# Kernel optimization log

Hardware: AMD Instinct MI355X
Metric: run time of the kernel (lower is better)

The kernel has to match this reference:

```python
import jax, jax.numpy as jnp
import numpy as np

D_MODEL = 1024
HEADS = 16
D_FF = 2048
EPS = 1e-6


def _ln(z, alpha, beta):
    # Faithful to the repo's (buggy-looking) LayerNorm:
    # mu = z - mean; sigma = std + eps; out = (z - mu/sigma)*alpha + beta
    mean = jnp.mean(z, axis=-1, keepdims=True)
    std = jnp.std(z, axis=-1, keepdims=True, ddof=1)  # torch.std is unbiased
    return (z - (z - mean) / (std + EPS)) * alpha + beta


def setup_inputs() -> dict:
    key = jax.random.key(0)
    ks = jax.random.split(key, 16)
    B, S, D = 8, 1024, D_MODEL
    s = 0.02
    inp = {
        "x": jax.random.normal(ks[0], (B, S, D), dtype=jnp.float32),
        "mask": jax.random.randint(ks[1], (B, S), 0, 2, dtype=jnp.int32),
        "Wq": jax.random.normal(ks[2], (D, D), dtype=jnp.float32) * s,
        "bq": jnp.zeros((D,), dtype=jnp.float32),
        "Wk": jax.random.normal(ks[3], (D, D), dtype=jnp.float32) * s,
        "bk": jnp.zeros((D,), dtype=jnp.float32),
        "Wv": jax.random.normal(ks[4], (D, D), dtype=jnp.float32) * s,
        "bv": jnp.zeros((D,), dtype=jnp.float32),
        "Wo": jax.random.normal(ks[5], (D, D), dtype=jnp.float32) * s,
        "bo": jnp.zeros((D,), dtype=jnp.float32),
        "W1": jax.random.normal(ks[6], (D_FF, D), dtype=jnp.float32) * s,
        "b1": jnp.zeros((D_FF,), dtype=jnp.float32),
        "W2": jax.random.normal(ks[7], (D, D_FF), dtype=jnp.float32) * s,
        "b2": jnp.zeros((D,), dtype=jnp.float32),
        "alpha1": jnp.ones((D,), dtype=jnp.float32),
        "beta1": jnp.zeros((D,), dtype=jnp.float32),
        "alpha2": jnp.ones((D,), dtype=jnp.float32),
        "beta2": jnp.zeros((D,), dtype=jnp.float32),
    }
    return inp


def reference(x, mask, Wq, bq, Wk, bk, Wv, bv, Wo, bo, W1, b1, W2, b2,
              alpha1, beta1, alpha2, beta2):
    B, S, D = x.shape
    H, dk = HEADS, D // HEADS
    # QKV projections (torch Linear: y = x @ W.T + b), split heads -> [B,H,S,dk]
    Q = (x @ Wq.T + bq).reshape(B, S, H, dk).transpose(0, 2, 1, 3)
    K = (x @ Wk.T + bk).reshape(B, S, H, dk).transpose(0, 2, 1, 3)
    V = (x @ Wv.T + bv).reshape(B, S, H, dk).transpose(0, 2, 1, 3)
    scores = jnp.einsum('bhqd,bhkd->bhqk', Q, K) / jnp.sqrt(jnp.float32(dk))
    # faithful mask broadcast: [B,1,S,1] over query rows
    m = mask[:, None, :, None]
    scores = jnp.where(m == 0, jnp.float32(-1e9), scores)
    A = jax.nn.softmax(scores, axis=-1)
    O = jnp.einsum('bhqk,bhkd->bhqd', A, V).transpose(0, 2, 1, 3).reshape(B, S, D)
    attn_out = O @ Wo.T + bo
    x1 = _ln(x + attn_out, alpha1, beta1)
    h = jax.nn.relu(x1 @ W1.T + b1)
    ff = h @ W2.T + b2
    return _ln(x1 + ff, alpha2, beta2)
```

## Files before the change

### kernel.cpp

```cpp
#include <hip/hip_runtime.h>
#include <cstdint>
#include <cstddef>

#define D_MODEL 1024
#define HEADS   16
#define DKH     64
#define D_FF    2048
#define SEQ     1024
#define BATCH   8
#define MROWS   (BATCH*SEQ)
#define LN_EPS  1e-6f

typedef __bf16 bh8 __attribute__((ext_vector_type(8)));
typedef float  f32x4 __attribute__((ext_vector_type(4)));
typedef unsigned short us8 __attribute__((ext_vector_type(8)));

__device__ __forceinline__ unsigned short f2bf(float f) {
  union { float f; unsigned int u; } c; c.f = f;
  unsigned int u = c.u;
  u = u + 0x7fffu + ((u >> 16) & 1u);
  return (unsigned short)(u >> 16);
}
__device__ __forceinline__ float bf2f(unsigned short h) {
  union { unsigned int u; float f; } c; c.u = ((unsigned int)h) << 16;
  return c.f;
}

__device__ __forceinline__ bh8 as_bh8(us8 v) { return __builtin_bit_cast(bh8, v); }

__device__ __forceinline__ void gl16(const unsigned short* g, unsigned short* l) {
  __builtin_amdgcn_global_load_lds(
      (const __attribute__((address_space(1))) unsigned int*)g,
      (__attribute__((address_space(3))) unsigned int*)l, 16, 0, 0);
}

__global__ void cast_bf16_k(const float* __restrict__ in, unsigned short* __restrict__ out, int n4) {
  int i = blockIdx.x * blockDim.x + threadIdx.x;
  if (i < n4) {
    float4 v = ((const float4*)in)[i];
    ushort4 o;
    o.x = f2bf(v.x); o.y = f2bf(v.y); o.z = f2bf(v.z); o.w = f2bf(v.w);
    ((ushort4*)out)[i] = o;
  }
}

__global__ void castw_k(const float* __restrict__ wq, const float* __restrict__ wk,
                        const float* __restrict__ wv, const float* __restrict__ wo,
                        const float* __restrict__ w1, const float* __restrict__ w2,
                        unsigned short* __restrict__ oqkv, unsigned short* __restrict__ oo,
                        unsigned short* __restrict__ o1, unsigned short* __restrict__ o2) {
  int i = blockIdx.x * blockDim.x + threadIdx.x;
  const int seg = i >> 18;
  const int loc = i & 262143;
  const float* src; unsigned short* dst; int il, ol;
  if (seg < 3)      { src = (seg == 0) ? wq : (seg == 1) ? wk : wv; dst = oqkv; il = loc; ol = seg * 262144 + loc; }
  else if (seg == 3){ src = wo; dst = oo; il = loc; ol = loc; }
  else if (seg < 6) { src = w1; dst = o1; il = (seg - 4) * 262144 + loc; ol = il; }
  else              { src = w2; dst = o2; il = (seg - 6) * 262144 + loc; ol = il; }
  float4 v = ((const float4*)src)[il];
  ushort4 o;
  o.x = f2bf(v.x); o.y = f2bf(v.y); o.z = f2bf(v.z); o.w = f2bf(v.w);
  ((ushort4*)dst)[ol] = o;
}

#define BM 128
#define BN 128
#define BK 64

template<int EPI>
__global__ __launch_bounds__(256)
void gemm_bt(const unsigned short* __restrict__ A, const unsigned short* __restrict__ Bw,
             const float* __restrict__ b0, const float* __restrict__ b1f,
             const float* __restrict__ b2f, const float* __restrict__ resid,
             void* __restrict__ out0, void* __restrict__ out1, void* __restrict__ out2,
             int M, int N, int K)
{
  __shared__ __align__(16) unsigned short As[2][BM * BK];
  __shared__ __align__(16) unsigned short Bs[2][BM * BK];

  const int tid  = threadIdx.x;
  const int lane = tid & 63;
  const int w    = tid >> 6;
  const int wr   = w >> 1;
  const int wc   = w & 1;
  const int l15  = lane & 15;
  const int l4   = lane >> 4;

  const int gx  = gridDim.x;
  const int nwg = gx * gridDim.y;
  int lin = blockIdx.y * gx + blockIdx.x;
  lin = (lin & 7) * (nwg >> 3) + (lin >> 3);
  const int brow = (lin / gx) * BM;
  const int bcol = (lin % gx) * BN;

  int rowj[4], offj[4];
  #pragma unroll
  for (int j = 0; j < 4; ++j) {
    const int c = tid + j * 256;
    rowj[j] = c >> 3;
    offj[j] = ((c & 7) ^ ((c >> 3) & 7)) * 8;
  }

  const unsigned short* Ag = A  + (size_t)brow * K;
  const unsigned short* Bg = Bw + (size_t)bcol * K;

  auto stage = [&](int bsel, int k0) {
    #pragma unroll
    for (int j = 0; j < 4; ++j)
      gl16(Ag + (size_t)rowj[j] * K + k0 + offj[j], &As[bsel][(tid + j * 256) * 8]);
    #pragma unroll
    for (int j = 0; j < 4; ++j)
      gl16(Bg + (size_t)rowj[j] * K + k0 + offj[j], &Bs[bsel][(tid + j * 256) * 8]);
  };

  const int NT = K / BK;
  stage(0, 0);
  stage(1, BK);

  f32x4 acc[4][4] = {};
  const int sw7 = l15 & 7;

  for (int t = 0; t < NT; ++t) {
    const int cur = t & 1;
    if (t + 1 < NT) { asm volatile("s_waitcnt vmcnt(8)" ::: "memory"); }
    else            { asm volatile("s_waitcnt vmcnt(0)" ::: "memory"); }
    __builtin_amdgcn_s_barrier();

    us8 aF[2][4], bF[2][4];
    #pragma unroll
    for (int h = 0; h < 2; ++h) {
      const int slot = ((h * 4 + l4) ^ sw7) * 8;
      #pragma unroll
      for (int mi = 0; mi < 4; ++mi)
        aF[h][mi] = *(const us8*)(&As[cur][(wr * 64 + mi * 16 + l15) * BK + slot]);
      #pragma unroll
      for (int ni = 0; ni < 4; ++ni)
        bF[h][ni] = *(const us8*)(&Bs[cur][(wc * 64 + ni * 16 + l15) * BK + slot]);
    }
    asm volatile("s_waitcnt lgkmcnt(0)" ::: "memory");
    __builtin_amdgcn_s_barrier();

    if (t + 2 < NT) stage(cur, (t + 2) * BK);

    #pragma unroll
    for (int h = 0; h < 2; ++h)
      #pragma unroll
      for (int mi = 0; mi < 4; ++mi)
        #pragma unroll
        for (int ni = 0; ni < 4; ++ni)
          acc[mi][ni] = __builtin_amdgcn_mfma_f32_16x16x32_bf16(
              as_bh8(aF[h][mi]), as_bh8(bF[h][ni]), acc[mi][ni], 0, 0, 0);
  }

  const int tt = bcol >> 10;
  #pragma unroll
  for (int mi = 0; mi < 4; ++mi) {
    #pragma unroll
    for (int ni = 0; ni < 4; ++ni) {
      const int gcol = bcol + wc * 64 + ni * 16 + l15;
      if (EPI == 4) {
        const int ccol = gcol & 1023;
        const float bv = ((tt == 0) ? b0 : (tt == 1) ? b1f : b2f)[ccol];
        const int grow0 = brow + wr * 64 + mi * 16 + l4 * 4;
        if (tt == 2) {
          const int bb = grow0 >> 10;
          const int s0 = grow0 & 1023;
          ushort4 pk;
          pk.x = f2bf(acc[mi][ni][0] + bv);
          pk.y = f2bf(acc[mi][ni][1] + bv);
          pk.z = f2bf(acc[mi][ni][2] + bv);
          pk.w = f2bf(acc[mi][ni][3] + bv);
          *(ushort4*)((unsigned short*)out2 + ((size_t)bb * D_MODEL + ccol) * SEQ + s0) = pk;
        } else {
          unsigned short* ob = (unsigned short*)(tt == 0 ? out0 : out1);
          #pragma unroll
          for (int v = 0; v < 4; ++v)
            ob[(size_t)(grow0 + v) * D_MODEL + ccol] = f2bf(acc[mi][ni][v] + bv);
        }
      } else {
        const float bv = b0[gcol];
        #pragma unroll
        for (int v = 0; v < 4; ++v) {
          const int grow = brow + wr * 64 + mi * 16 + l4 * 4 + v;
          float val = acc[mi][ni][v] + bv;
          if (EPI == 3) val = fmaxf(val, 0.0f);
          if (EPI == 2) {
            val += resid[(size_t)grow * N + gcol];
            ((float*)out0)[(size_t)grow * N + gcol] = val;
          } else {
            ((unsigned short*)out0)[(size_t)grow * N + gcol] = f2bf(val);
          }
        }
      }
    }
  }
}

__global__ __launch_bounds__(256)
void attn_k(const unsigned short* __restrict__ Q, const unsigned short* __restrict__ Kb,
            const unsigned short* __restrict__ Vt, const int* __restrict__ mask,
            unsigned short* __restrict__ O)
{
  __shared__ __align__(16) unsigned short Ks[2][64][64];
  __shared__ __align__(16) unsigned short Vs[2][64][64];
  __shared__ __align__(16) unsigned short Pl[4][16][88];

  const int bid = (blockIdx.x & 7) * 256 + (blockIdx.x >> 3);
  const int qc = bid & 15;
  const int h  = (bid >> 4) & 15;
  const int b  = bid >> 8;
  const int q0 = qc * 64;

  const int tid  = threadIdx.x;
  const int lane = tid & 63;
  const int w    = tid >> 6;
  const int l15  = lane & 15;
  const int l4   = lane >> 4;

  const int c0 = tid, c1 = tid + 256;
  const int kr0 = c0 >> 3, ke0 = ((c0 & 7) ^ (kr0 & 7)) * 8;
  const int kr1 = c1 >> 3, ke1 = ((c1 & 7) ^ (kr1 & 7)) * 8;

  const unsigned short* Kbase = Kb + ((size_t)b * SEQ) * D_MODEL + h * DKH;
  const unsigned short* Vbase = Vt + ((size_t)b * D_MODEL + h * DKH) * SEQ;

  const unsigned short* qp = Q + ((size_t)(b * SEQ + q0 + w * 16 + l15)) * D_MODEL + h * DKH + l4 * 8;
  const float qs = mask[b * SEQ + q0 + w * 16 + l15] ? 0.18033688011112042f : 0.0f;
  us8 q0r = *(const us8*)qp;
  us8 q1r = *(const us8*)(qp + 32);
  us8 q0s, q1s;
  #pragma unroll
  for (int j = 0; j < 8; ++j) {
    q0s[j] = f2bf(bf2f(q0r[j]) * qs);
    q1s[j] = f2bf(bf2f(q1r[j]) * qs);
  }
  const bh8 aQ0 = as_bh8(q0s);
  const bh8 aQ1 = as_bh8(q1s);

  float l[4] = {0.f, 0.f, 0.f, 0.f};
  f32x4 oacc[4] = {};

  gl16(Kbase + (size_t)kr0 * D_MODEL + ke0, &Ks[0][0][0] + c0 * 8);
  gl16(Kbase + (size_t)kr1 * D_MODEL + ke1, &Ks[0][0][0] + c1 * 8);
  gl16(Vbase + (size_t)kr0 * SEQ + ke0,     &Vs[0][0][0] + c0 * 8);
  gl16(Vbase + (size_t)kr1 * SEQ + ke1,     &Vs[0][0][0] + c1 * 8);
  __syncthreads();

  for (int t = 0; t < 16; ++t) {
    const int cur = t & 1;
    if (t < 15) {
      const int kv = (t + 1) * 64;
      gl16(Kbase + (size_t)(kv + kr0) * D_MODEL + ke0, &Ks[cur ^ 1][0][0] + c0 * 8);
      gl16(Kbase + (size_t)(kv + kr1) * D_MODEL + ke1, &Ks[cur ^ 1][0][0] + c1 * 8);
      gl16(Vbase + (size_t)kr0 * SEQ + kv + ke0,       &Vs[cur ^ 1][0][0] + c0 * 8);
      gl16(Vbase + (size_t)kr1 * SEQ + kv + ke1,       &Vs[cur ^ 1][0][0] + c1 * 8);
    }

    f32x4 s[4];
    #pragma unroll
    for (int kt = 0; kt < 4; ++kt) {
      const int row = kt * 16 + l15;
      const int swz = l15 & 7;
      bh8 bK0 = as_bh8(*(const us8*)(&Ks[cur][row][(l4 ^ swz) * 8]));
      bh8 bK1 = as_bh8(*(const us8*)(&Ks[cur][row][((4 + l4) ^ swz) * 8]));
      f32x4 t0 = {0.f, 0.f, 0.f, 0.f};
      t0 = __builtin_amdgcn_mfma_f32_16x16x32_bf16(aQ0, bK0, t0, 0, 0, 0);
      t0 = __builtin_amdgcn_mfma_f32_16x16x32_bf16(aQ1, bK1, t0, 0, 0, 0);
      s[kt] = t0;
    }

    #pragma unroll
    for (int v = 0; v < 4; ++v) {
      float ls = 0.f;
      #pragma unroll
      for (int kt = 0; kt < 4; ++kt) {
        float e = __builtin_amdgcn_exp2f(s[kt][v]);
        s[kt][v] = e;
        ls += e;
      }
      l[v] += ls;
    }

    #pragma unroll
    for (int kt = 0; kt < 4; ++kt)
      #pragma unroll
      for (int v = 0; v < 4; ++v)
        Pl[w][l4 * 4 + v][kt * 16 + l15] = f2bf(s[kt][v]);

    #pragma unroll
    for (int ks = 0; ks < 2; ++ks) {
      bh8 aP = as_bh8(*(const us8*)(&Pl[w][l15][ks * 32 + l4 * 8]));
      #pragma unroll
      for (int ds = 0; ds < 4; ++ds) {
        const int row = ds * 16 + l15;
        bh8 bV = as_bh8(*(const us8*)(&Vs[cur][row][((ks * 4 + l4) ^ (l15 & 7)) * 8]));
        oacc[ds] = __builtin_amdgcn_mfma_f32_16x16x32_bf16(aP, bV, oacc[ds], 0, 0, 0);
      }
    }
    __syncthreads();
  }

  #pragma unroll
  for (int v = 0; v < 4; ++v) {
    float lv = l[v];
    #pragma unroll
    for (int d = 1; d < 16; d <<= 1) lv += __shfl_xor(lv, d, 64);
    const float inv = 1.0f / lv;
    const int q = q0 + w * 16 + l4 * 4 + v;
    #pragma unroll
    for (int ds = 0; ds < 4; ++ds)
      O[((size_t)(b * SEQ + q)) * D_MODEL + h * DKH + ds * 16 + l15] =
          f2bf(oacc[ds][v] * inv);
  }
}

template<bool WBF>
__global__ __launch_bounds__(256)
void ln_k(const float* __restrict__ z, const float* __restrict__ alpha,
          const float* __restrict__ beta, float* __restrict__ yf,
          unsigned short* __restrict__ yb)
{
  const int row = blockIdx.x;
  const int tid = threadIdx.x;
  const float4 v = ((const float4*)(z + (size_t)row * D_MODEL))[tid];
  float s  = v.x + v.y + v.z + v.w;
  float ss = v.x * v.x + v.y * v.y + v.z * v.z + v.w * v.w;
  #pragma unroll
  for (int d = 1; d < 64; d <<= 1) {
    s  += __shfl_xor(s, d, 64);
    ss += __shfl_xor(ss, d, 64);
  }
  __shared__ float red[8];
  const int w = tid >> 6;
  if ((tid & 63) == 0) { red[w * 2] = s; red[w * 2 + 1] = ss; }
  __syncthreads();
  const float S  = red[0] + red[2] + red[4] + red[6];
  const float SS = red[1] + red[3] + red[5] + red[7];
  const float mean = S * (1.0f / 1024.0f);
  float var = (SS - 1024.0f * mean * mean) * (1.0f / 1023.0f);
  var = fmaxf(var, 0.0f);
  const float invd = 1.0f / (sqrtf(var) + LN_EPS);

  const float4 a  = ((const float4*)alpha)[tid];
  const float4 be = ((const float4*)beta)[tid];
  float4 y;
  y.x = (v.x - (v.x - mean) * invd) * a.x + be.x;
  y.y = (v.y - (v.y - mean) * invd) * a.y + be.y;
  y.z = (v.z - (v.z - mean) * invd) * a.z + be.z;
  y.w = (v.w - (v.w - mean) * invd) * a.w + be.w;
  ((float4*)(yf + (size_t)row * D_MODEL))[tid] = y;
  if (WBF) {
    ushort4 pk;
    pk.x = f2bf(y.x); pk.y = f2bf(y.y); pk.z = f2bf(y.z); pk.w = f2bf(y.w);
    ((ushort4*)(yb + (size_t)row * D_MODEL))[tid] = pk;
  }
}

extern "C" void kernel_launch(void* const* d_in, const int* in_sizes, int n_in,
                              void* d_out, int out_size, void* d_ws, size_t ws_size,
                              hipStream_t stream) {
  const float* x    = (const float*)d_in[0];
  const int*   mask = (const int*)d_in[1];
  const float* Wq = (const float*)d_in[2];  const float* bq = (const float*)d_in[3];
  const float* Wk = (const float*)d_in[4];  const float* bk = (const float*)d_in[5];
  const float* Wv = (const float*)d_in[6];  const float* bv = (const float*)d_in[7];
  const float* Wo = (const float*)d_in[8];  const float* bo = (const float*)d_in[9];
  const float* W1 = (const float*)d_in[10]; const float* b1 = (const float*)d_in[11];
  const float* W2 = (const float*)d_in[12]; const float* b2 = (const float*)d_in[13];
  const float* alpha1 = (const float*)d_in[14]; const float* beta1 = (const float*)d_in[15];
  const float* alpha2 = (const float*)d_in[16]; const float* beta2 = (const float*)d_in[17];
  (void)in_sizes; (void)n_in; (void)out_size; (void)ws_size;

  char* ws = (char*)d_ws;
  const size_t MB = (size_t)1 << 20;
  unsigned short* xb    = (unsigned short*)(ws + 0 * MB);
  unsigned short* Wqkvb = (unsigned short*)(ws + 16 * MB);
  unsigned short* Wob   = (unsigned short*)(ws + 22 * MB);
  unsigned short* W1b   = (unsigned short*)(ws + 24 * MB);
  unsigned short* W2b   = (unsigned short*)(ws + 28 * MB);
  unsigned short* Qb    = (unsigned short*)(ws + 32 * MB);
  unsigned short* Kb2   = (unsigned short*)(ws + 48 * MB);
  unsigned short* Vt    = (unsigned short*)(ws + 64 * MB);
  unsigned short* Ob    = (unsigned short*)(ws + 80 * MB);
  float*          zf    = (float*)(ws + 96 * MB);
  float*          x1f   = (float*)(ws + 128 * MB);
  unsigned short* x1b   = (unsigned short*)(ws + 160 * MB);
  unsigned short* hb    = Qb;

  cast_bf16_k<<<8192, 256, 0, stream>>>(x, xb, MROWS * D_MODEL / 4);
  castw_k<<<8192, 256, 0, stream>>>(Wq, Wk, Wv, Wo, W1, W2, Wqkvb, Wob, W1b, W2b);

  gemm_bt<4><<<dim3(24, 64), 256, 0, stream>>>(xb, Wqkvb, bq, bk, bv, nullptr,
                                               Qb, Kb2, Vt, MROWS, 3072, D_MODEL);

  attn_k<<<BATCH * HEADS * (SEQ / 64), 256, 0, stream>>>(Qb, Kb2, Vt, mask, Ob);

  gemm_bt<2><<<dim3(8, 64), 256, 0, stream>>>(Ob, Wob, bo, nullptr, nullptr, x,
                                              zf, nullptr, nullptr, MROWS, D_MODEL, D_MODEL);
  ln_k<true><<<MROWS, 256, 0, stream>>>(zf, alpha1, beta1, x1f, x1b);

  gemm_bt<3><<<dim3(16, 64), 256, 0, stream>>>(x1b, W1b, b1, nullptr, nullptr, nullptr,
                                               hb, nullptr, nullptr, MROWS, D_FF, D_MODEL);
  gemm_bt<2><<<dim3(8, 64), 256, 0, stream>>>(hb, W2b, b2, nullptr, nullptr, x1f,
                                              zf, nullptr, nullptr, MROWS, D_MODEL, D_FF);

  ln_k<false><<<MROWS, 256, 0, stream>>>(zf, alpha2, beta2, (float*)d_out, nullptr);
}
```

Baseline: 296.7 us.

## Prefetch KV two tiles ahead and load LDS fragments into registers early

The attention kernel now stages the first two K/V tiles up front and, inside the loop, waits with a partial vmcnt so that one tile's global loads stay in flight. Each iteration first copies all K and V fragments for the current tile from LDS into registers, then hits a barrier and reuses that buffer for the tile two steps ahead. This gives global loads more time to land, and the MFMA work runs from registers. In exchange each iteration has two barriers and uses more registers for the fragments, and the vmcnt count relies on gl16 being exactly four outstanding loads per stage.

```diff
diff --git a/kernel.cpp b/kernel.cpp
--- a/kernel.cpp
+++ b/kernel.cpp
@@ -240,32 +240,49 @@
   float l[4] = {0.f, 0.f, 0.f, 0.f};
   f32x4 oacc[4] = {};
 
-  gl16(Kbase + (size_t)kr0 * D_MODEL + ke0, &Ks[0][0][0] + c0 * 8);
-  gl16(Kbase + (size_t)kr1 * D_MODEL + ke1, &Ks[0][0][0] + c1 * 8);
-  gl16(Vbase + (size_t)kr0 * SEQ + ke0,     &Vs[0][0][0] + c0 * 8);
-  gl16(Vbase + (size_t)kr1 * SEQ + ke1,     &Vs[0][0][0] + c1 * 8);
-  __syncthreads();
+  auto stageKV = [&](int bsel, int kv) {
+    gl16(Kbase + (size_t)(kv + kr0) * D_MODEL + ke0, &Ks[bsel][0][0] + c0 * 8);
+    gl16(Kbase + (size_t)(kv + kr1) * D_MODEL + ke1, &Ks[bsel][0][0] + c1 * 8);
+    gl16(Vbase + (size_t)kr0 * SEQ + kv + ke0,       &Vs[bsel][0][0] + c0 * 8);
+    gl16(Vbase + (size_t)kr1 * SEQ + kv + ke1,       &Vs[bsel][0][0] + c1 * 8);
+  };
+
+  stageKV(0, 0);
+  stageKV(1, 64);
+
+  const int swz = l15 & 7;
 
   for (int t = 0; t < 16; ++t) {
     const int cur = t & 1;
-    if (t < 15) {
-      const int kv = (t + 1) * 64;
-      gl16(Kbase + (size_t)(kv + kr0) * D_MODEL + ke0, &Ks[cur ^ 1][0][0] + c0 * 8);
-      gl16(Kbase + (size_t)(kv + kr1) * D_MODEL + ke1, &Ks[cur ^ 1][0][0] + c1 * 8);
-      gl16(Vbase + (size_t)kr0 * SEQ + kv + ke0,       &Vs[cur ^ 1][0][0] + c0 * 8);
-      gl16(Vbase + (size_t)kr1 * SEQ + kv + ke1,       &Vs[cur ^ 1][0][0] + c1 * 8);
-    }
-
-    f32x4 s[4];
+    if (t + 1 < 16) { asm volatile("s_waitcnt vmcnt(4)" ::: "memory"); }
+    else            { asm volatile("s_waitcnt vmcnt(0)" ::: "memory"); }
+    __builtin_amdgcn_s_barrier();
+
+    us8 kF[4][2], vF[2][4];
     #pragma unroll
     for (int kt = 0; kt < 4; ++kt) {
       const int row = kt * 16 + l15;
-      const int swz = l15 & 7;
-      bh8 bK0 = as_bh8(*(const us8*)(&Ks[cur][row][(l4 ^ swz) * 8]));
-      bh8 bK1 = as_bh8(*(const us8*)(&Ks[cur][row][((4 + l4) ^ swz) * 8]));
+      kF[kt][0] = *(const us8*)(&Ks[cur][row][(l4 ^ swz) * 8]);
+      kF[kt][1] = *(const us8*)(&Ks[cur][row][((4 + l4) ^ swz) * 8]);
+    }
+    #pragma unroll
+    for (int ks = 0; ks < 2; ++ks)
+      #pragma unroll
+      for (int ds = 0; ds < 4; ++ds) {
+        const int row = ds * 16 + l15;
+        vF[ks][ds] = *(const us8*)(&Vs[cur][row][((ks * 4 + l4) ^ swz) * 8]);
+      }
+    asm volatile("s_waitcnt lgkmcnt(0)" ::: "memory");
+    __builtin_amdgcn_s_barrier();
+
+    if (t + 2 < 16) stageKV(cur, (t + 2) * 64);
+
+    f32x4 s[4];
+    #pragma unroll
+    for (int kt = 0; kt < 4; ++kt) {
       f32x4 t0 = {0.f, 0.f, 0.f, 0.f};
-      t0 = __builtin_amdgcn_mfma_f32_16x16x32_bf16(aQ0, bK0, t0, 0, 0, 0);
-      t0 = __builtin_amdgcn_mfma_f32_16x16x32_bf16(aQ1, bK1, t0, 0, 0, 0);
+      t0 = __builtin_amdgcn_mfma_f32_16x16x32_bf16(aQ0, as_bh8(kF[kt][0]), t0, 0, 0, 0);
+      t0 = __builtin_amdgcn_mfma_f32_16x16x32_bf16(aQ1, as_bh8(kF[kt][1]), t0, 0, 0, 0);
       s[kt] = t0;
     }
 
@@ -291,13 +308,9 @@
     for (int ks = 0; ks < 2; ++ks) {
       bh8 aP = as_bh8(*(const us8*)(&Pl[w][l15][ks * 32 + l4 * 8]));
       #pragma unroll
-      for (int ds = 0; ds < 4; ++ds) {
-        const int row = ds * 16 + l15;
-        bh8 bV = as_bh8(*(const us8*)(&Vs[cur][row][((ks * 4 + l4) ^ (l15 & 7)) * 8]));
-        oacc[ds] = __builtin_amdgcn_mfma_f32_16x16x32_bf16(aP, bV, oacc[ds], 0, 0, 0);
-      }
-    }
-    __syncthreads();
+      for (int ds = 0; ds < 4; ++ds)
+        oacc[ds] = __builtin_amdgcn_mfma_f32_16x16x32_bf16(aP, as_bh8(vF[ks][ds]), oacc[ds], 0, 0, 0);
+    }
   }
 
   #pragma unroll
```

After: 283.1 us. 1.05x faster.
